# Performance work log

Measured on AMD Instinct MI355X. Metric: run time of the kernel, lower is better.

Reference implementation:

```python
import jax, jax.numpy as jnp
import numpy as np

N_NODES = 50000
N_EDGES = 1600000
NFEAT, NHID, NCLASS = 512, 256, 64


def _mpnn_layer(x, src, dst, W, b, num_nodes):
    # linear transform then mean aggregation over incoming edges (incl. self loops)
    h = x @ W + b                      # [N, out]
    msg = h[src]                       # gather along edges [E+N, out]
    agg = jax.ops.segment_sum(msg, dst, num_segments=num_nodes)
    ones = jnp.ones((src.shape[0],), dtype=x.dtype)
    cnt = jax.ops.segment_sum(ones, dst, num_segments=num_nodes)
    return agg / jnp.maximum(cnt, 1.0)[:, None]


def setup_inputs() -> dict:
    key = jax.random.key(0)
    k1, k2, k3, k4, k5, k6 = jax.random.split(key, 6)
    x = jax.random.normal(k1, (N_NODES, NFEAT), dtype=jnp.float32)
    edge_index = jax.random.randint(k2, (2, N_EDGES), 0, N_NODES, dtype=jnp.int64)
    W1 = jax.random.normal(k3, (NFEAT, NHID), dtype=jnp.float32) * (1.0 / np.sqrt(NFEAT))
    b1 = jax.random.normal(k4, (NHID,), dtype=jnp.float32) * 0.01
    W2 = jax.random.normal(k5, (NHID, NCLASS), dtype=jnp.float32) * (1.0 / np.sqrt(NHID))
    b2 = jax.random.normal(k6, (NCLASS,), dtype=jnp.float32) * 0.01
    return {"x": x, "edge_index": edge_index, "W1": W1, "b1": b1, "W2": W2, "b2": b2}


def reference(x, edge_index, W1, b1, W2, b2):
    n = x.shape[0]
    # add self loops (done once per layer in the original; edge set identical)
    loops = jnp.arange(n, dtype=edge_index.dtype)
    src = jnp.concatenate([edge_index[0], loops])
    dst = jnp.concatenate([edge_index[1], loops])

    h = _mpnn_layer(x, src, dst, W1, b1, n)
    h = jax.nn.relu(h)
    # dropout is identity at inference
    h = _mpnn_layer(h, src, dst, W2, b2, n)
    return jax.nn.log_softmax(h, axis=1)
```

## Files before the change

kernel.cpp:

```cpp
#include <hip/hip_runtime.h>
#include <math.h>

#define NN 50000
#define NE 1600000
#define NF 512
#define NH 256
#define NC 64
#define CAP 96
#define NBKT 196
#define BCAP 9728
#define G1_BLOCKS 391
#define P1_BLOCKS 392

typedef short bf16x8 __attribute__((ext_vector_type(8)));
typedef float f32x4  __attribute__((ext_vector_type(4)));
typedef float f32x2  __attribute__((ext_vector_type(2)));

__device__ __forceinline__ float bf2f(unsigned short u) {
    return __uint_as_float(((unsigned)u) << 16);
}
__device__ __forceinline__ unsigned short f2bf(float f) {
    unsigned u = __float_as_uint(f);
    unsigned r = (u + 0x7FFF + ((u >> 16) & 1)) >> 16;
    return (unsigned short)r;
}

__device__ __forceinline__ unsigned char f2e4m3(float f) {
#if __has_builtin(__builtin_amdgcn_cvt_pk_fp8_f32)
    int v = __builtin_amdgcn_cvt_pk_fp8_f32(f, f, 0, false);
    return (unsigned char)(v & 0xff);
#else
    unsigned u = __float_as_uint(f);
    unsigned s = (u >> 31) << 7;
    float a = fabsf(f);
    if (a >= 448.f) return (unsigned char)(s | 0x7E);
    int e32 = (int)((u >> 23) & 0xff) - 127;
    if (e32 < -6) {
        int m = (int)rintf(a * 512.f);
        return (unsigned char)(s | m);
    }
    unsigned mant = u & 0x7fffff;
    unsigned keep = mant >> 20;
    unsigned rest = mant & 0xfffff;
    if (rest > 0x80000 || (rest == 0x80000 && (keep & 1))) keep++;
    int e8 = e32 + 7;
    if (keep == 8) { keep = 0; e8++; }
    if (e8 >= 16 || (e8 == 15 && keep == 7)) return (unsigned char)(s | 0x7E);
    return (unsigned char)(s | (e8 << 3) | keep);
#endif
}

__device__ __forceinline__ void dec4(unsigned int u, float& x0, float& x1, float& x2, float& x3) {
#if __has_builtin(__builtin_amdgcn_cvt_pk_f32_fp8)
    f32x2 lo = __builtin_amdgcn_cvt_pk_f32_fp8(u, false);
    f32x2 hi = __builtin_amdgcn_cvt_pk_f32_fp8(u, true);
    x0 = lo[0]; x1 = lo[1]; x2 = hi[0]; x3 = hi[1];
#else
    float r[4];
    #pragma unroll
    for (int i = 0; i < 4; ++i) {
        unsigned b = (u >> (8 * i)) & 0xff;
        unsigned s = (b >> 7) & 1, e = (b >> 3) & 15, m = b & 7;
        float v = e ? __uint_as_float(((e + 120u) << 23) | (m << 20))
                    : (float)m * 0.001953125f;
        r[i] = s ? -v : v;
    }
    x0 = r[0]; x1 = r[1]; x2 = r[2]; x3 = r[3];
#endif
}

__global__ __launch_bounds__(256)
void prep(const float* __restrict__ W1, const float* __restrict__ W2,
          unsigned short* __restrict__ w1t, unsigned short* __restrict__ w2t,
          const int* __restrict__ ei, int2* __restrict__ pairs, int* __restrict__ cursor,
          unsigned char* __restrict__ h1f, unsigned short* __restrict__ h2b) {
    __shared__ int bcnt[NBKT];
    __shared__ int bpos[NBKT];
    const int b = blockIdx.x;
    const int t = threadIdx.x;
    if (b < NF) {
        w1t[(size_t)t * NF + b] = f2bf(W1[(size_t)b * NH + t]);
        return;
    }
    if (b < NF + NH) {
        const int k = b - NF;
        if (t < NC) w2t[(size_t)t * NH + k] = f2bf(W2[(size_t)k * NC + t]);
        return;
    }
    if (b == NF + NH + P1_BLOCKS) {
        if (t < 64) reinterpret_cast<unsigned int*>(h1f)[(size_t)NN * 64 + t] = 0u;
        if (t < 32) reinterpret_cast<unsigned int*>(h2b)[(size_t)NN * 32 + t] = 0u;
        return;
    }
    const int fb = b - NF - NH;
    const int base = fb * 4096;
    for (int i = t; i < NBKT; i += 256) bcnt[i] = 0;
    __syncthreads();
    int ds[16], ss[16];
    #pragma unroll
    for (int k = 0; k < 16; ++k) {
        const int e = base + k * 256 + t;
        if (e < NE) {
            ds[k] = ei[NE + e];
            ss[k] = ei[e];
            atomicAdd(&bcnt[ds[k] >> 8], 1);
        } else ds[k] = -1;
    }
    __syncthreads();
    for (int i = t; i < NBKT; i += 256) bpos[i] = atomicAdd(&cursor[i], bcnt[i]);
    __syncthreads();
    #pragma unroll
    for (int k = 0; k < 16; ++k) {
        if (ds[k] >= 0) {
            const int bkt = ds[k] >> 8;
            const int p = atomicAdd(&bcnt[bkt], -1) - 1;
            const int g = bpos[bkt] + p;
            if (g < BCAP) {
                int2 v; v.x = ds[k]; v.y = ss[k];
                pairs[(size_t)bkt * BCAP + g] = v;
            }
        }
    }
}

__global__ __launch_bounds__(512)
void gemm1_fill(const float* __restrict__ A, const unsigned short* __restrict__ BT,
                const float* __restrict__ bias, unsigned char* __restrict__ C,
                const int2* __restrict__ pairs, const int* __restrict__ cursor,
                int* __restrict__ deg, int* __restrict__ csr) {
    __shared__ __align__(16) unsigned char smem[34816];
    __shared__ int ldeg[256];
    const int tid = threadIdx.x;

    if (blockIdx.x >= G1_BLOCKS) {
        const int fb = blockIdx.x - G1_BLOCKS;
        const int nb = fb * 256;
        if (tid < 256) ldeg[tid] = 0;
        __syncthreads();
        int cnt = cursor[fb];
        if (cnt > BCAP) cnt = BCAP;
        const int2* pb = pairs + (size_t)fb * BCAP;
        for (int i = tid; i < cnt; i += 512) {
            const int2 e = pb[i];
            const int p = atomicAdd(&ldeg[e.x & 255], 1);
            if (p < CAP) csr[(size_t)e.x * CAP + p] = e.y;
        }
        __syncthreads();
        if (tid < 256) {
            const int node = nb + tid;
            if (node < NN) {
                const int d = ldeg[tid];
                deg[node] = d;
                const int dc = min(d, CAP);
                const int pd = min((dc + 15) & ~15, CAP);
                for (int p = dc; p < pd; ++p) csr[(size_t)node * CAP + p] = NN;
            }
        }
        return;
    }

    unsigned short (*As)[40] = reinterpret_cast<unsigned short (*)[40]>(smem);
    unsigned short (*Bs)[40] = reinterpret_cast<unsigned short (*)[40]>(smem + 10240);
    const int w    = tid >> 6, lane = tid & 63;
    const int wr   = w >> 2,   wc   = w & 3;
    const int bm   = blockIdx.x * 128;
    const int rl   = lane & 15;
    const int ko   = (lane >> 4) * 8;

    f32x4 acc[4][4] = {};

    for (int k0 = 0; k0 < NF; k0 += 32) {
        {
            const int row = tid >> 2;
            const int kc  = (tid & 3) * 8;
            const int gr  = bm + row;
            float4 v0 = make_float4(0.f, 0.f, 0.f, 0.f), v1 = v0;
            if (gr < NN) {
                const float4* p = reinterpret_cast<const float4*>(A + (size_t)gr * NF + k0 + kc);
                v0 = p[0]; v1 = p[1];
            }
            bf16x8 pk;
            pk[0] = (short)f2bf(v0.x); pk[1] = (short)f2bf(v0.y);
            pk[2] = (short)f2bf(v0.z); pk[3] = (short)f2bf(v0.w);
            pk[4] = (short)f2bf(v1.x); pk[5] = (short)f2bf(v1.y);
            pk[6] = (short)f2bf(v1.z); pk[7] = (short)f2bf(v1.w);
            *reinterpret_cast<bf16x8*>(&As[row][kc]) = pk;
        }
        {
            const int row = tid >> 1;
            const int kc  = (tid & 1) * 16;
            const bf16x8* p = reinterpret_cast<const bf16x8*>(BT + (size_t)row * NF + k0 + kc);
            *reinterpret_cast<bf16x8*>(&Bs[row][kc])     = p[0];
            *reinterpret_cast<bf16x8*>(&Bs[row][kc + 8]) = p[1];
        }
        __syncthreads();

        bf16x8 af[4], bfr[4];
        #pragma unroll
        for (int m = 0; m < 4; ++m)
            af[m] = *reinterpret_cast<const bf16x8*>(&As[wr * 64 + m * 16 + rl][ko]);
        #pragma unroll
        for (int n = 0; n < 4; ++n)
            bfr[n] = *reinterpret_cast<const bf16x8*>(&Bs[wc * 64 + n * 16 + rl][ko]);
        #pragma unroll
        for (int m = 0; m < 4; ++m)
            #pragma unroll
            for (int n = 0; n < 4; ++n)
                acc[m][n] = __builtin_amdgcn_mfma_f32_16x16x32_bf16(af[m], bfr[n], acc[m][n], 0, 0, 0);
        __syncthreads();
    }

    unsigned char (*ct)[272] = reinterpret_cast<unsigned char (*)[272]>(smem);
    float bv[4];
    #pragma unroll
    for (int n = 0; n < 4; ++n) bv[n] = bias[wc * 64 + n * 16 + rl];
    #pragma unroll
    for (int m = 0; m < 4; ++m) {
        #pragma unroll
        for (int j = 0; j < 4; ++j) {
            const int rloc = wr * 64 + m * 16 + (lane >> 4) * 4 + j;
            #pragma unroll
            for (int n = 0; n < 4; ++n)
                ct[rloc][wc * 64 + n * 16 + rl] = f2e4m3(acc[m][n][j] + bv[n]);
        }
    }
    __syncthreads();
    {
        const int row = tid >> 2;
        const int seg = (tid & 3) * 64;
        const int gr  = bm + row;
        if (gr < NN) {
            const uint4* s = reinterpret_cast<const uint4*>(&ct[row][seg]);
            uint4* d = reinterpret_cast<uint4*>(C + (size_t)gr * NH + seg);
            d[0] = s[0]; d[1] = s[1]; d[2] = s[2]; d[3] = s[3];
        }
    }
}

__global__ __launch_bounds__(256)
void gemm2_mfma(const unsigned short* __restrict__ A, const unsigned short* __restrict__ BT,
                const float* __restrict__ bias, unsigned short* __restrict__ C) {
    __shared__ unsigned short As[128][40];
    __shared__ unsigned short Bs[64][40];
    const int tid = threadIdx.x;
    const int w = tid >> 6, lane = tid & 63;
    const int bm = blockIdx.x * 128;
    const int rl = lane & 15, ko = (lane >> 4) * 8;

    f32x4 acc[2][4] = {};

    for (int k0 = 0; k0 < NH; k0 += 32) {
        #pragma unroll
        for (int h = 0; h < 2; ++h) {
            const int c = tid + h * 256;
            const int row = c >> 2, kc = (c & 3) * 8;
            const int gr = bm + row;
            bf16x8 v = {};
            if (gr < NN) v = *reinterpret_cast<const bf16x8*>(A + (size_t)gr * NH + k0 + kc);
            *reinterpret_cast<bf16x8*>(&As[row][kc]) = v;
        }
        {
            const int row = tid >> 2, kc = (tid & 3) * 8;
            *reinterpret_cast<bf16x8*>(&Bs[row][kc]) =
                *reinterpret_cast<const bf16x8*>(BT + (size_t)row * NH + k0 + kc);
        }
        __syncthreads();

        bf16x8 af[2], bfr[4];
        #pragma unroll
        for (int m = 0; m < 2; ++m)
            af[m] = *reinterpret_cast<const bf16x8*>(&As[w * 32 + m * 16 + rl][ko]);
        #pragma unroll
        for (int n = 0; n < 4; ++n)
            bfr[n] = *reinterpret_cast<const bf16x8*>(&Bs[n * 16 + rl][ko]);
        #pragma unroll
        for (int m = 0; m < 2; ++m)
            #pragma unroll
            for (int n = 0; n < 4; ++n)
                acc[m][n] = __builtin_amdgcn_mfma_f32_16x16x32_bf16(af[m], bfr[n], acc[m][n], 0, 0, 0);
        __syncthreads();
    }

    float bv[4];
    #pragma unroll
    for (int n = 0; n < 4; ++n) bv[n] = bias[n * 16 + rl];
    #pragma unroll
    for (int m = 0; m < 2; ++m) {
        #pragma unroll
        for (int j = 0; j < 4; ++j) {
            const int row = bm + w * 32 + m * 16 + (lane >> 4) * 4 + j;
            if (row < NN) {
                #pragma unroll
                for (int n = 0; n < 4; ++n)
                    C[(size_t)row * NC + n * 16 + rl] = f2bf(acc[m][n][j] + bv[n]);
            }
        }
    }
}

__global__ __launch_bounds__(256)
void agg_relu(const unsigned char* __restrict__ hf, const int* __restrict__ deg,
              const int* __restrict__ csr, unsigned short* __restrict__ o) {
    const int node = blockIdx.x * 4 + (threadIdx.x >> 6);
    const int lane = threadIdx.x & 63;
    if (node >= NN) return;
    const int dcnt = min(deg[node], CAP);
    const int pad = (dcnt + 15) & ~15;
    const unsigned int* hfu = reinterpret_cast<const unsigned int*>(hf);
    const size_t loff = lane;

    float a0, a1, a2, a3;
    dec4(hfu[(size_t)node * 64 + loff], a0, a1, a2, a3);

    #define LDA(EE) hfu[(size_t)csr[EE] * 64 + loff]
    #define ACCA(U) { float b0,b1,b2,b3; dec4(U,b0,b1,b2,b3); a0+=b0; a1+=b1; a2+=b2; a3+=b3; }
    int e = node * CAP;
    const int eend = e + pad;
    if (pad > 0) {
        unsigned u0=LDA(e+0),u1=LDA(e+1),u2=LDA(e+2),u3=LDA(e+3),
                 u4=LDA(e+4),u5=LDA(e+5),u6=LDA(e+6),u7=LDA(e+7),
                 u8=LDA(e+8),u9=LDA(e+9),u10=LDA(e+10),u11=LDA(e+11),
                 u12=LDA(e+12),u13=LDA(e+13),u14=LDA(e+14),u15=LDA(e+15);
        e += 16;
        for (; e < eend; e += 16) {
            unsigned t;
            t=LDA(e+0);  ACCA(u0)  u0=t;
            t=LDA(e+1);  ACCA(u1)  u1=t;
            t=LDA(e+2);  ACCA(u2)  u2=t;
            t=LDA(e+3);  ACCA(u3)  u3=t;
            t=LDA(e+4);  ACCA(u4)  u4=t;
            t=LDA(e+5);  ACCA(u5)  u5=t;
            t=LDA(e+6);  ACCA(u6)  u6=t;
            t=LDA(e+7);  ACCA(u7)  u7=t;
            t=LDA(e+8);  ACCA(u8)  u8=t;
            t=LDA(e+9);  ACCA(u9)  u9=t;
            t=LDA(e+10); ACCA(u10) u10=t;
            t=LDA(e+11); ACCA(u11) u11=t;
            t=LDA(e+12); ACCA(u12) u12=t;
            t=LDA(e+13); ACCA(u13) u13=t;
            t=LDA(e+14); ACCA(u14) u14=t;
            t=LDA(e+15); ACCA(u15) u15=t;
        }
        ACCA(u0) ACCA(u1) ACCA(u2) ACCA(u3) ACCA(u4) ACCA(u5) ACCA(u6) ACCA(u7)
        ACCA(u8) ACCA(u9) ACCA(u10) ACCA(u11) ACCA(u12) ACCA(u13) ACCA(u14) ACCA(u15)
    }
    #undef LDA
    #undef ACCA

    const float inv = 1.0f / (float)(dcnt + 1);
    ushort4 r;
    r.x = f2bf(fmaxf(a0 * inv, 0.f));
    r.y = f2bf(fmaxf(a1 * inv, 0.f));
    r.z = f2bf(fmaxf(a2 * inv, 0.f));
    r.w = f2bf(fmaxf(a3 * inv, 0.f));
    *reinterpret_cast<ushort4*>(o + (size_t)node * NH + lane * 4) = r;
}

__global__ __launch_bounds__(256)
void agg2_softmax(const unsigned short* __restrict__ h2, const int* __restrict__ deg,
                  const int* __restrict__ csr, float* __restrict__ out) {
    const int node = blockIdx.x * 8 + (threadIdx.x >> 5);
    const int l = threadIdx.x & 31;
    if (node >= NN) return;
    const int dcnt = min(deg[node], CAP);
    const int pad = (dcnt + 15) & ~15;
    const unsigned int* h2u = reinterpret_cast<const unsigned int*>(h2);

    unsigned int su = h2u[(size_t)node * 32 + l];
    float a0 = bf2f((unsigned short)(su & 0xffff));
    float a1 = bf2f((unsigned short)(su >> 16));

    #define LDB(EE) h2u[(size_t)csr[EE] * 32 + l]
    #define ACCB(U) { a0 += bf2f((unsigned short)((U) & 0xffff)); a1 += bf2f((unsigned short)((U) >> 16)); }
    int e = node * CAP;
    const int eend = e + pad;
    if (pad > 0) {
        unsigned u0=LDB(e+0),u1=LDB(e+1),u2=LDB(e+2),u3=LDB(e+3),
                 u4=LDB(e+4),u5=LDB(e+5),u6=LDB(e+6),u7=LDB(e+7),
                 u8=LDB(e+8),u9=LDB(e+9),u10=LDB(e+10),u11=LDB(e+11),
                 u12=LDB(e+12),u13=LDB(e+13),u14=LDB(e+14),u15=LDB(e+15);
        e += 16;
        for (; e < eend; e += 16) {
            unsigned t;
            t=LDB(e+0);  ACCB(u0)  u0=t;
            t=LDB(e+1);  ACCB(u1)  u1=t;
            t=LDB(e+2);  ACCB(u2)  u2=t;
            t=LDB(e+3);  ACCB(u3)  u3=t;
            t=LDB(e+4);  ACCB(u4)  u4=t;
            t=LDB(e+5);  ACCB(u5)  u5=t;
            t=LDB(e+6);  ACCB(u6)  u6=t;
            t=LDB(e+7);  ACCB(u7)  u7=t;
            t=LDB(e+8);  ACCB(u8)  u8=t;
            t=LDB(e+9);  ACCB(u9)  u9=t;
            t=LDB(e+10); ACCB(u10) u10=t;
            t=LDB(e+11); ACCB(u11) u11=t;
            t=LDB(e+12); ACCB(u12) u12=t;
            t=LDB(e+13); ACCB(u13) u13=t;
            t=LDB(e+14); ACCB(u14) u14=t;
            t=LDB(e+15); ACCB(u15) u15=t;
        }
        ACCB(u0) ACCB(u1) ACCB(u2) ACCB(u3) ACCB(u4) ACCB(u5) ACCB(u6) ACCB(u7)
        ACCB(u8) ACCB(u9) ACCB(u10) ACCB(u11) ACCB(u12) ACCB(u13) ACCB(u14) ACCB(u15)
    }
    #undef LDB
    #undef ACCB

    const float inv = 1.0f / (float)(dcnt + 1);
    a0 *= inv; a1 *= inv;

    float m = fmaxf(a0, a1);
    #pragma unroll
    for (int o = 16; o > 0; o >>= 1) m = fmaxf(m, __shfl_xor(m, o));
    float s = expf(a0 - m) + expf(a1 - m);
    #pragma unroll
    for (int o = 16; o > 0; o >>= 1) s += __shfl_xor(s, o);
    const float lg = logf(s);
    float2 r;
    r.x = a0 - m - lg;
    r.y = a1 - m - lg;
    *reinterpret_cast<float2*>(out + (size_t)node * NC + l * 2) = r;
}

extern "C" void kernel_launch(void* const* d_in, const int* in_sizes, int n_in,
                              void* d_out, int out_size, void* d_ws, size_t ws_size,
                              hipStream_t stream) {
    const float* x  = (const float*)d_in[0];
    const int*   ei = (const int*)d_in[1];
    const float* W1 = (const float*)d_in[2];
    const float* b1 = (const float*)d_in[3];
    const float* W2 = (const float*)d_in[4];
    const float* b2 = (const float*)d_in[5];
    float* out = (float*)d_out;

    char* ws = (char*)d_ws;
    unsigned short* hr     = (unsigned short*)(ws);
    unsigned char*  h1f    = (unsigned char*)(ws + 25600000);
    unsigned short* h2b    = (unsigned short*)(ws + 38400256);
    unsigned short* w1t    = (unsigned short*)(ws + 44800512);
    unsigned short* w2t    = (unsigned short*)(ws + 45062656);
    int*            deg    = (int*)(ws + 45095424);
    int*            csr    = (int*)(ws + 45295424);
    int2*           pairs  = (int2*)(ws + 64495424);
    int*            cursor = (int*)(ws + 79748928);

    hipMemsetAsync(cursor, 0, NBKT * sizeof(int), stream);

    prep<<<NF + NH + P1_BLOCKS + 1, 256, 0, stream>>>(W1, W2, w1t, w2t, ei, pairs, cursor, h1f, h2b);

    gemm1_fill<<<G1_BLOCKS + NBKT, 512, 0, stream>>>(x, w1t, b1, h1f, pairs, cursor, deg, csr);

    agg_relu<<<(NN + 3) / 4, 256, 0, stream>>>(h1f, deg, csr, hr);

    gemm2_mfma<<<(NN + 127) / 128, 256, 0, stream>>>(hr, w2t, b2, h2b);

    agg2_softmax<<<(NN + 7) / 8, 256, 0, stream>>>(h2b, deg, csr, out);
}
```

Baseline: 149.6 us.

## Double-buffer LDS tiles in gemm1 with register prefetch of next K slice

The first GEMM now keeps two LDS buffers for the A and B tiles and loads the next K slice into registers before computing on the current one. It then writes the next slice into the alternate buffer, so each K step needs one barrier instead of two and global load latency can overlap with MFMA work. Shared memory per block grows from about 35KB to 61KB, which may lower occupancy and could slow the CSR-fill blocks that share this kernel.

```diff
diff --git a/kernel.cpp b/kernel.cpp
--- a/kernel.cpp
+++ b/kernel.cpp
@@ -128,7 +128,7 @@
                 const float* __restrict__ bias, unsigned char* __restrict__ C,
                 const int2* __restrict__ pairs, const int* __restrict__ cursor,
                 int* __restrict__ deg, int* __restrict__ csr) {
-    __shared__ __align__(16) unsigned char smem[34816];
+    __shared__ __align__(16) unsigned char smem[61440];
     __shared__ int ldeg[256];
     const int tid = threadIdx.x;
 
@@ -159,56 +159,83 @@
         return;
     }
 
-    unsigned short (*As)[40] = reinterpret_cast<unsigned short (*)[40]>(smem);
-    unsigned short (*Bs)[40] = reinterpret_cast<unsigned short (*)[40]>(smem + 10240);
     const int w    = tid >> 6, lane = tid & 63;
     const int wr   = w >> 2,   wc   = w & 3;
     const int bm   = blockIdx.x * 128;
     const int rl   = lane & 15;
     const int ko   = (lane >> 4) * 8;
 
+    const int arow = tid >> 2, akc = (tid & 3) * 8;
+    const int gr   = bm + arow;
+    const bool aval = gr < NN;
+    const float4* ap = reinterpret_cast<const float4*>(A + (size_t)min(gr, NN - 1) * NF + akc);
+    const int brow = tid >> 1, bkc = (tid & 1) * 16;
+    const bf16x8* bp = reinterpret_cast<const bf16x8*>(BT + (size_t)brow * NF + bkc);
+
     f32x4 acc[4][4] = {};
 
-    for (int k0 = 0; k0 < NF; k0 += 32) {
-        {
-            const int row = tid >> 2;
-            const int kc  = (tid & 3) * 8;
-            const int gr  = bm + row;
-            float4 v0 = make_float4(0.f, 0.f, 0.f, 0.f), v1 = v0;
-            if (gr < NN) {
-                const float4* p = reinterpret_cast<const float4*>(A + (size_t)gr * NF + k0 + kc);
-                v0 = p[0]; v1 = p[1];
-            }
-            bf16x8 pk;
-            pk[0] = (short)f2bf(v0.x); pk[1] = (short)f2bf(v0.y);
-            pk[2] = (short)f2bf(v0.z); pk[3] = (short)f2bf(v0.w);
-            pk[4] = (short)f2bf(v1.x); pk[5] = (short)f2bf(v1.y);
-            pk[6] = (short)f2bf(v1.z); pk[7] = (short)f2bf(v1.w);
-            *reinterpret_cast<bf16x8*>(&As[row][kc]) = pk;
-        }
-        {
-            const int row = tid >> 1;
-            const int kc  = (tid & 1) * 16;
-            const bf16x8* p = reinterpret_cast<const bf16x8*>(BT + (size_t)row * NF + k0 + kc);
-            *reinterpret_cast<bf16x8*>(&Bs[row][kc])     = p[0];
-            *reinterpret_cast<bf16x8*>(&Bs[row][kc + 8]) = p[1];
-        }
-        __syncthreads();
-
-        bf16x8 af[4], bfr[4];
-        #pragma unroll
-        for (int m = 0; m < 4; ++m)
-            af[m] = *reinterpret_cast<const bf16x8*>(&As[wr * 64 + m * 16 + rl][ko]);
-        #pragma unroll
-        for (int n = 0; n < 4; ++n)
-            bfr[n] = *reinterpret_cast<const bf16x8*>(&Bs[wc * 64 + n * 16 + rl][ko]);
-        #pragma unroll
-        for (int m = 0; m < 4; ++m)
-            #pragma unroll
-            for (int n = 0; n < 4; ++n)
-                acc[m][n] = __builtin_amdgcn_mfma_f32_16x16x32_bf16(af[m], bfr[n], acc[m][n], 0, 0, 0);
-        __syncthreads();
-    }
+    #define AS_AT(c) (reinterpret_cast<unsigned short (*)[40]>(smem + (c) * 10240))
+    #define BS_AT(c) (reinterpret_cast<unsigned short (*)[40]>(smem + 20480 + (c) * 20480))
+
+    #define STAGE_WRITE(cbuf, V0, V1, B0, B1) {                                   \
+        bf16x8 pk;                                                                \
+        pk[0] = (short)f2bf((V0).x); pk[1] = (short)f2bf((V0).y);                 \
+        pk[2] = (short)f2bf((V0).z); pk[3] = (short)f2bf((V0).w);                 \
+        pk[4] = (short)f2bf((V1).x); pk[5] = (short)f2bf((V1).y);                 \
+        pk[6] = (short)f2bf((V1).z); pk[7] = (short)f2bf((V1).w);                 \
+        *reinterpret_cast<bf16x8*>(&AS_AT(cbuf)[arow][akc]) = pk;                 \
+        *reinterpret_cast<bf16x8*>(&BS_AT(cbuf)[brow][bkc])     = (B0);           \
+        *reinterpret_cast<bf16x8*>(&BS_AT(cbuf)[brow][bkc + 8]) = (B1);           \
+    }
+
+    #define COMPUTE(cbuf) {                                                       \
+        unsigned short (*Asc)[40] = AS_AT(cbuf);                                  \
+        unsigned short (*Bsc)[40] = BS_AT(cbuf);                                  \
+        bf16x8 af[4], bfr[4];                                                     \
+        _Pragma("unroll")                                                         \
+        for (int m = 0; m < 4; ++m)                                               \
+            af[m] = *reinterpret_cast<const bf16x8*>(&Asc[wr * 64 + m * 16 + rl][ko]); \
+        _Pragma("unroll")                                                         \
+        for (int n = 0; n < 4; ++n)                                               \
+            bfr[n] = *reinterpret_cast<const bf16x8*>(&Bsc[wc * 64 + n * 16 + rl][ko]); \
+        _Pragma("unroll")                                                         \
+        for (int m = 0; m < 4; ++m)                                               \
+            _Pragma("unroll")                                                     \
+            for (int n = 0; n < 4; ++n)                                           \
+                acc[m][n] = __builtin_amdgcn_mfma_f32_16x16x32_bf16(af[m], bfr[n], acc[m][n], 0, 0, 0); \
+    }
+
+    {
+        float4 v0 = make_float4(0.f, 0.f, 0.f, 0.f), v1 = v0;
+        if (aval) { v0 = ap[0]; v1 = ap[1]; }
+        bf16x8 b0 = bp[0], b1 = bp[1];
+        STAGE_WRITE(0, v0, v1, b0, b1)
+    }
+    __syncthreads();
+
+    int cur = 0;
+    for (int s = 0; s < 15; ++s) {
+        float4 v0 = make_float4(0.f, 0.f, 0.f, 0.f), v1 = v0;
+        if (aval) { v0 = ap[(s + 1) * 8]; v1 = ap[(s + 1) * 8 + 1]; }
+        bf16x8 b0 = bp[(s + 1) * 4], b1 = bp[(s + 1) * 4 + 1];
+        __builtin_amdgcn_sched_barrier(0);
+
+        COMPUTE(cur)
+        __builtin_amdgcn_sched_barrier(0);
+
+        STAGE_WRITE(cur ^ 1, v0, v1, b0, b1)
+        asm volatile("s_waitcnt lgkmcnt(0)" ::: "memory");
+        __builtin_amdgcn_sched_barrier(0);
+        __builtin_amdgcn_s_barrier();
+        cur ^= 1;
+    }
+    COMPUTE(cur)
+    __syncthreads();
+
+    #undef AS_AT
+    #undef BS_AT
+    #undef STAGE_WRITE
+    #undef COMPUTE
 
     unsigned char (*ct)[272] = reinterpret_cast<unsigned char (*)[272]>(smem);
     float bv[4];
@@ -228,10 +255,10 @@
     {
         const int row = tid >> 2;
         const int seg = (tid & 3) * 64;
-        const int gr  = bm + row;
-        if (gr < NN) {
+        const int grr = bm + row;
+        if (grr < NN) {
             const uint4* s = reinterpret_cast<const uint4*>(&ct[row][seg]);
-            uint4* d = reinterpret_cast<uint4*>(C + (size_t)gr * NH + seg);
+            uint4* d = reinterpret_cast<uint4*>(C + (size_t)grr * NH + seg);
             d[0] = s[0]; d[1] = s[1]; d[2] = s[2]; d[3] = s[3];
         }
     }
```

Measured after the change: 149.3 us. No clear change (-0.2%).

## Load GEMM MFMA fragments directly from global memory, dropping LDS staging

Applied to the files above, without the earlier changes.

The first-layer GEMM no longer stages A and B tiles through shared memory with two barriers per k-step. Each lane now reads its own MFMA fragments straight from global memory, converting A from fp32 to bf16 in registers, and the k-loop is unrolled by two. This removes the LDS round-trip and the block-wide synchronisation. In exchange, each A row is fetched redundantly by the four column waves and each B row by the two row waves, so more traffic goes to the L2/L1 caches.

```diff
diff --git a/kernel.cpp b/kernel.cpp
--- a/kernel.cpp
+++ b/kernel.cpp
@@ -159,55 +159,48 @@
         return;
     }
 
-    unsigned short (*As)[40] = reinterpret_cast<unsigned short (*)[40]>(smem);
-    unsigned short (*Bs)[40] = reinterpret_cast<unsigned short (*)[40]>(smem + 10240);
     const int w    = tid >> 6, lane = tid & 63;
     const int wr   = w >> 2,   wc   = w & 3;
     const int bm   = blockIdx.x * 128;
     const int rl   = lane & 15;
     const int ko   = (lane >> 4) * 8;
 
+    const float* apm[4];
+    #pragma unroll
+    for (int m = 0; m < 4; ++m) {
+        const int r = min(bm + wr * 64 + m * 16 + rl, NN - 1);
+        apm[m] = A + (size_t)r * NF + ko;
+    }
+    const unsigned short* bpn[4];
+    #pragma unroll
+    for (int n = 0; n < 4; ++n)
+        bpn[n] = BT + (size_t)(wc * 64 + n * 16 + rl) * NF + ko;
+
     f32x4 acc[4][4] = {};
 
-    for (int k0 = 0; k0 < NF; k0 += 32) {
-        {
-            const int row = tid >> 2;
-            const int kc  = (tid & 3) * 8;
-            const int gr  = bm + row;
-            float4 v0 = make_float4(0.f, 0.f, 0.f, 0.f), v1 = v0;
-            if (gr < NN) {
-                const float4* p = reinterpret_cast<const float4*>(A + (size_t)gr * NF + k0 + kc);
-                v0 = p[0]; v1 = p[1];
-            }
+    #pragma unroll 2
+    for (int ks = 0; ks < NF / 32; ++ks) {
+        const int k0 = ks * 32;
+        bf16x8 af[4], bfr[4];
+        #pragma unroll
+        for (int m = 0; m < 4; ++m) {
+            const float4 v0 = *reinterpret_cast<const float4*>(apm[m] + k0);
+            const float4 v1 = *reinterpret_cast<const float4*>(apm[m] + k0 + 4);
             bf16x8 pk;
             pk[0] = (short)f2bf(v0.x); pk[1] = (short)f2bf(v0.y);
             pk[2] = (short)f2bf(v0.z); pk[3] = (short)f2bf(v0.w);
             pk[4] = (short)f2bf(v1.x); pk[5] = (short)f2bf(v1.y);
             pk[6] = (short)f2bf(v1.z); pk[7] = (short)f2bf(v1.w);
-            *reinterpret_cast<bf16x8*>(&As[row][kc]) = pk;
-        }
-        {
-            const int row = tid >> 1;
-            const int kc  = (tid & 1) * 16;
-            const bf16x8* p = reinterpret_cast<const bf16x8*>(BT + (size_t)row * NF + k0 + kc);
-            *reinterpret_cast<bf16x8*>(&Bs[row][kc])     = p[0];
-            *reinterpret_cast<bf16x8*>(&Bs[row][kc + 8]) = p[1];
-        }
-        __syncthreads();
-
-        bf16x8 af[4], bfr[4];
-        #pragma unroll
-        for (int m = 0; m < 4; ++m)
-            af[m] = *reinterpret_cast<const bf16x8*>(&As[wr * 64 + m * 16 + rl][ko]);
+            af[m] = pk;
+        }
         #pragma unroll
         for (int n = 0; n < 4; ++n)
-            bfr[n] = *reinterpret_cast<const bf16x8*>(&Bs[wc * 64 + n * 16 + rl][ko]);
+            bfr[n] = *reinterpret_cast<const bf16x8*>(bpn[n] + k0);
         #pragma unroll
         for (int m = 0; m < 4; ++m)
             #pragma unroll
             for (int n = 0; n < 4; ++n)
                 acc[m][n] = __builtin_amdgcn_mfma_f32_16x16x32_bf16(af[m], bfr[n], acc[m][n], 0, 0, 0);
-        __syncthreads();
     }
 
     unsigned char (*ct)[272] = reinterpret_cast<unsigned char (*)[272]>(smem);
```

Result: slower. 205.3 us (+37.2%).
